# Performance work log

Hardware: AMD Instinct MI355X
Metric: run time of the kernel (lower is better)

The kernel has to match this reference:

```python
import jax, jax.numpy as jnp
import numpy as np

def setup_inputs() -> dict:
    key = jax.random.key(0)
    x = jax.random.normal(key, (4096, 3, 64, 64), dtype=jnp.float32)
    return {"x": x}

def reference(x):
    # x: [N, C=3, H, W]; attention runs over the N dim with feature dim H*W
    N, C, H, W = x.shape
    out = x.reshape(N, C, H * W)          # [N, 3, HW]
    q, k, v = out[:, 0], out[:, 1], out[:, 2]  # each [N, HW]
    dp = (q @ k.T) * 0.5                  # [N, N]
    attn = jax.nn.softmax(dp, axis=-1)
    # dropout omitted (eval-mode / deterministic reference)
    return attn @ v                       # [N, HW]
```

## Files before the change

kernel.cpp:

```cpp
#include <hip/hip_runtime.h>
#include <hip/hip_bf16.h>
#include <cstdint>

#define N 4096
#define ROWSTRIDE 12288

typedef __attribute__((ext_vector_type(8))) _Float16 half8;
typedef __attribute__((ext_vector_type(4))) _Float16 half4v;
typedef __attribute__((ext_vector_type(4))) float floatx4;

__global__ __launch_bounds__(256) void pack_qk(const float* __restrict__ x,
                                               _Float16* __restrict__ qh,
                                               _Float16* __restrict__ kh) {
    const size_t tid = (size_t)blockIdx.x * 256 + threadIdx.x;
    const int i  = (int)(tid >> 10);
    const int c4 = (int)(tid & 1023);
    const float4* xr = (const float4*)(x + (size_t)i * ROWSTRIDE);
    float4 q = xr[c4];
    float4 k = xr[1024 + c4];
    half4v qo = {(_Float16)(q.x * 0.5f), (_Float16)(q.y * 0.5f),
                 (_Float16)(q.z * 0.5f), (_Float16)(q.w * 0.5f)};
    half4v ko = {(_Float16)k.x, (_Float16)k.y, (_Float16)k.z, (_Float16)k.w};
    *(half4v*)(qh + tid * 4) = qo;
    *(half4v*)(kh + tid * 4) = ko;
}

__global__ __launch_bounds__(256) void transpose_v(const float* __restrict__ x,
                                                   _Float16* __restrict__ vt) {
    __shared__ float tile[32][33];
    const int j0 = blockIdx.x * 32;
    const int d0 = blockIdx.y * 32;
    const int t  = threadIdx.x;
    const int r  = t >> 3;
    const int c4 = t & 7;
    const float4 val = *(const float4*)(x + (size_t)(j0 + r) * ROWSTRIDE + 8192 + d0 + c4 * 4);
    tile[r][c4 * 4 + 0] = val.x;
    tile[r][c4 * 4 + 1] = val.y;
    tile[r][c4 * 4 + 2] = val.z;
    tile[r][c4 * 4 + 3] = val.w;
    __syncthreads();
    half4v o = {(_Float16)tile[c4 * 4 + 0][r], (_Float16)tile[c4 * 4 + 1][r],
                (_Float16)tile[c4 * 4 + 2][r], (_Float16)tile[c4 * 4 + 3][r]};
    *(half4v*)(vt + (size_t)(d0 + r) * N + j0 + c4 * 4) = o;
}

#define GL2LDS(g, l)                                                                     \
    __builtin_amdgcn_global_load_lds((const __attribute__((address_space(1))) void*)(g), \
                                     (__attribute__((address_space(3))) void*)(l), 16, 0, 0)

__global__ __launch_bounds__(512, 2) void gemm_nt256(const _Float16* __restrict__ A,
                                                     const _Float16* __restrict__ Bt,
                                                     float* __restrict__ C) {
    __shared__ _Float16 lds[65536];
    const int t    = threadIdx.x;
    const int wave = t >> 6;
    const int lane = t & 63;
    const int wr   = wave >> 2;
    const int wc   = wave & 3;

    const int orig = blockIdx.y * 16 + blockIdx.x;
    const int wg   = (orig & 7) * 32 + (orig >> 3);
    const int rowBase = (wg >> 4) * 256;
    const int colBase = (wg & 15) * 256;

    floatx4 acc[8][4] = {};

    const int sRow = t >> 2;
    const int sCg  = (t & 3) ^ ((t >> 3) & 3);
    const _Float16* gA = A  + (size_t)(rowBase + sRow) * N + sCg * 8;
    const _Float16* gB = Bt + (size_t)(colBase + sRow) * N + sCg * 8;
    const int ldsW = wave * 512;

    const int fr   = lane & 15;
    const int quad = lane >> 4;
    const int swc  = quad ^ ((fr >> 1) & 3);
    const int rdA  = (wr * 128 + fr) * 32 + swc * 8;
    const int rdB  = (wc * 64 + fr) * 32 + swc * 8;

#define STAGE(regOff, g, kOff)                                                  \
    do {                                                                        \
        GL2LDS((g) + (kOff), &lds[(regOff) + ldsW]);                            \
        GL2LDS((g) + (kOff) + (size_t)128 * N, &lds[(regOff) + 4096 + ldsW]);   \
    } while (0)

    STAGE(0, gA, 0);
    STAGE(8192, gB, 0);
    STAGE(16384, gA, 32);
    STAGE(24576, gB, 32);
    asm volatile("s_waitcnt vmcnt(4)" ::: "memory");
    __builtin_amdgcn_s_barrier();

    for (int kt = 0; kt < 63; ++kt) {
        const int rb = (kt & 1) * 32768;
        const int sb = rb ^ 32768;
        const int kNext = (kt + 1) * 64;
#pragma unroll
        for (int kh = 0; kh < 2; ++kh) {
            const int rA = rb + kh * 16384;
            const int rB = rA + 8192;
            half8 af[4], bf[4];
#pragma unroll
            for (int nt = 0; nt < 4; ++nt) bf[nt] = *(const half8*)&lds[rB + nt * 512 + rdB];
#pragma unroll
            for (int mt = 0; mt < 4; ++mt) af[mt] = *(const half8*)&lds[rA + mt * 512 + rdA];
            STAGE(sb + kh * 16384, gA, kNext + kh * 32);
            __builtin_amdgcn_s_barrier();
            asm volatile("s_waitcnt lgkmcnt(0)" ::: "memory");
            __builtin_amdgcn_s_setprio(1);
#pragma unroll
            for (int mt = 0; mt < 4; ++mt)
#pragma unroll
                for (int nt = 0; nt < 4; ++nt)
                    acc[mt][nt] = __builtin_amdgcn_mfma_f32_16x16x32_f16(af[mt], bf[nt],
                                                                         acc[mt][nt], 0, 0, 0);
            __builtin_amdgcn_s_setprio(0);
            __builtin_amdgcn_s_barrier();
#pragma unroll
            for (int mt = 0; mt < 4; ++mt) af[mt] = *(const half8*)&lds[rA + (mt + 4) * 512 + rdA];
            STAGE(sb + kh * 16384 + 8192, gB, kNext + kh * 32);
            asm volatile("s_waitcnt vmcnt(4)" ::: "memory");
            __builtin_amdgcn_s_barrier();
            asm volatile("s_waitcnt lgkmcnt(0)" ::: "memory");
            __builtin_amdgcn_s_setprio(1);
#pragma unroll
            for (int mt = 0; mt < 4; ++mt)
#pragma unroll
                for (int nt = 0; nt < 4; ++nt)
                    acc[mt + 4][nt] = __builtin_amdgcn_mfma_f32_16x16x32_f16(af[mt], bf[nt],
                                                                             acc[mt + 4][nt], 0, 0, 0);
            __builtin_amdgcn_s_setprio(0);
            __builtin_amdgcn_s_barrier();
        }
    }

    {
        const int rb = 32768;
#pragma unroll
        for (int kh = 0; kh < 2; ++kh) {
            const int rA = rb + kh * 16384;
            const int rB = rA + 8192;
            half8 af[4], bf[4];
#pragma unroll
            for (int nt = 0; nt < 4; ++nt) bf[nt] = *(const half8*)&lds[rB + nt * 512 + rdB];
#pragma unroll
            for (int mt = 0; mt < 4; ++mt) af[mt] = *(const half8*)&lds[rA + mt * 512 + rdA];
            __builtin_amdgcn_s_barrier();
            asm volatile("s_waitcnt lgkmcnt(0)" ::: "memory");
            __builtin_amdgcn_s_setprio(1);
#pragma unroll
            for (int mt = 0; mt < 4; ++mt)
#pragma unroll
                for (int nt = 0; nt < 4; ++nt)
                    acc[mt][nt] = __builtin_amdgcn_mfma_f32_16x16x32_f16(af[mt], bf[nt],
                                                                         acc[mt][nt], 0, 0, 0);
            __builtin_amdgcn_s_setprio(0);
            __builtin_amdgcn_s_barrier();
#pragma unroll
            for (int mt = 0; mt < 4; ++mt) af[mt] = *(const half8*)&lds[rA + (mt + 4) * 512 + rdA];
            if (kh == 0) asm volatile("s_waitcnt vmcnt(0)" ::: "memory");
            __builtin_amdgcn_s_barrier();
            asm volatile("s_waitcnt lgkmcnt(0)" ::: "memory");
            __builtin_amdgcn_s_setprio(1);
#pragma unroll
            for (int mt = 0; mt < 4; ++mt)
#pragma unroll
                for (int nt = 0; nt < 4; ++nt)
                    acc[mt + 4][nt] = __builtin_amdgcn_mfma_f32_16x16x32_f16(af[mt], bf[nt],
                                                                             acc[mt + 4][nt], 0, 0, 0);
            __builtin_amdgcn_s_setprio(0);
            __builtin_amdgcn_s_barrier();
        }
    }

#pragma unroll
    for (int mt = 0; mt < 8; ++mt) {
#pragma unroll
        for (int nt = 0; nt < 4; ++nt) {
#pragma unroll
            for (int r = 0; r < 4; ++r) {
                const int row = rowBase + wr * 128 + mt * 16 + quad * 4 + r;
                const int col = colBase + wc * 64 + nt * 16 + fr;
                C[(size_t)row * N + col] = acc[mt][nt][r];
            }
        }
    }
#undef STAGE
}

__global__ __launch_bounds__(256) void softmax_rows(const float* __restrict__ S,
                                                    _Float16* __restrict__ P) {
    const int row = blockIdx.x;
    const int t   = threadIdx.x;
    const float4* Sr = (const float4*)(S + (size_t)row * N);

    float4 v[4];
    float lmax = -3.0e38f;
#pragma unroll
    for (int r = 0; r < 4; ++r) {
        v[r] = Sr[t + 256 * r];
        lmax = fmaxf(lmax, fmaxf(fmaxf(v[r].x, v[r].y), fmaxf(v[r].z, v[r].w)));
    }
#pragma unroll
    for (int off = 32; off; off >>= 1) lmax = fmaxf(lmax, __shfl_xor(lmax, off, 64));
    __shared__ float redm[4], reds[4];
    const int wave = t >> 6, lane = t & 63;
    if (lane == 0) redm[wave] = lmax;
    __syncthreads();
    const float m = fmaxf(fmaxf(redm[0], redm[1]), fmaxf(redm[2], redm[3]));

    float lsum = 0.f;
#pragma unroll
    for (int r = 0; r < 4; ++r) {
        v[r].x = __expf(v[r].x - m);
        v[r].y = __expf(v[r].y - m);
        v[r].z = __expf(v[r].z - m);
        v[r].w = __expf(v[r].w - m);
        lsum += (v[r].x + v[r].y) + (v[r].z + v[r].w);
    }
#pragma unroll
    for (int off = 32; off; off >>= 1) lsum += __shfl_xor(lsum, off, 64);
    if (lane == 0) reds[wave] = lsum;
    __syncthreads();
    const float inv = 1.0f / (((reds[0] + reds[1]) + (reds[2] + reds[3])));

#pragma unroll
    for (int r = 0; r < 4; ++r) {
        half4v o = {(_Float16)(v[r].x * inv), (_Float16)(v[r].y * inv),
                    (_Float16)(v[r].z * inv), (_Float16)(v[r].w * inv)};
        *(half4v*)(P + (size_t)row * N + (t + 256 * r) * 4) = o;
    }
}

extern "C" void kernel_launch(void* const* d_in, const int* in_sizes, int n_in,
                              void* d_out, int out_size, void* d_ws, size_t ws_size,
                              hipStream_t stream) {
    const float* x = (const float*)d_in[0];
    float* out     = (float*)d_out;
    char* ws       = (char*)d_ws;

    _Float16* qh = (_Float16*)(ws);
    _Float16* kh = (_Float16*)(ws + (32ull << 20));
    _Float16* vt = (_Float16*)(ws + (64ull << 20));
    float*    S  = (float*)   (ws + (96ull << 20));
    _Float16* P  = qh;

    pack_qk     <<<16384, 256, 0, stream>>>(x, qh, kh);
    transpose_v <<<dim3(128, 128), 256, 0, stream>>>(x, vt);
    gemm_nt256  <<<dim3(16, 16), 512, 0, stream>>>(qh, kh, S);
    softmax_rows<<<4096, 256, 0, stream>>>(S, P);
    gemm_nt256  <<<dim3(16, 16), 512, 0, stream>>>(P, vt, out);
}
```

Baseline: 546.7 us.

## Drop post-MFMA barriers in GEMM and widen pack/transpose stores to half8

Removes the workgroup barrier after each MFMA block in both the main and tail loops of the GEMM. The aim is to cut synchronisation stalls so waves can begin the next fragment loads and staging sooner. The pack_qk and transpose_v kernels are also changed to handle twice the data per thread and write 16-byte half8 stores, which halves their grid sizes. The risk is an LDS race: the pipeline's buffer reuse may have depended on the removed barriers.

Measured after the change: 529.5 us. 1.03x faster.

```diff
diff --git a/kernel.cpp b/kernel.cpp
--- a/kernel.cpp
+++ b/kernel.cpp
@@ -13,35 +13,45 @@
                                                _Float16* __restrict__ qh,
                                                _Float16* __restrict__ kh) {
     const size_t tid = (size_t)blockIdx.x * 256 + threadIdx.x;
-    const int i  = (int)(tid >> 10);
-    const int c4 = (int)(tid & 1023);
+    const int i  = (int)(tid >> 9);
+    const int c8 = (int)(tid & 511);
     const float4* xr = (const float4*)(x + (size_t)i * ROWSTRIDE);
-    float4 q = xr[c4];
-    float4 k = xr[1024 + c4];
-    half4v qo = {(_Float16)(q.x * 0.5f), (_Float16)(q.y * 0.5f),
-                 (_Float16)(q.z * 0.5f), (_Float16)(q.w * 0.5f)};
-    half4v ko = {(_Float16)k.x, (_Float16)k.y, (_Float16)k.z, (_Float16)k.w};
-    *(half4v*)(qh + tid * 4) = qo;
-    *(half4v*)(kh + tid * 4) = ko;
+    float4 qa = xr[c8 * 2], qb = xr[c8 * 2 + 1];
+    float4 ka = xr[1024 + c8 * 2], kb = xr[1024 + c8 * 2 + 1];
+    half8 qo = {(_Float16)(qa.x * 0.5f), (_Float16)(qa.y * 0.5f),
+                (_Float16)(qa.z * 0.5f), (_Float16)(qa.w * 0.5f),
+                (_Float16)(qb.x * 0.5f), (_Float16)(qb.y * 0.5f),
+                (_Float16)(qb.z * 0.5f), (_Float16)(qb.w * 0.5f)};
+    half8 ko = {(_Float16)ka.x, (_Float16)ka.y, (_Float16)ka.z, (_Float16)ka.w,
+                (_Float16)kb.x, (_Float16)kb.y, (_Float16)kb.z, (_Float16)kb.w};
+    *(half8*)(qh + (size_t)i * N + c8 * 8) = qo;
+    *(half8*)(kh + (size_t)i * N + c8 * 8) = ko;
 }
 
 __global__ __launch_bounds__(256) void transpose_v(const float* __restrict__ x,
                                                    _Float16* __restrict__ vt) {
-    __shared__ float tile[32][33];
+    __shared__ float tile[32][65];
     const int j0 = blockIdx.x * 32;
-    const int d0 = blockIdx.y * 32;
+    const int d0 = blockIdx.y * 64;
     const int t  = threadIdx.x;
-    const int r  = t >> 3;
-    const int c4 = t & 7;
-    const float4 val = *(const float4*)(x + (size_t)(j0 + r) * ROWSTRIDE + 8192 + d0 + c4 * 4);
-    tile[r][c4 * 4 + 0] = val.x;
-    tile[r][c4 * 4 + 1] = val.y;
-    tile[r][c4 * 4 + 2] = val.z;
-    tile[r][c4 * 4 + 3] = val.w;
+#pragma unroll
+    for (int it = 0; it < 2; ++it) {
+        const int r  = it * 16 + (t >> 4);
+        const int c4 = t & 15;
+        const float4 val =
+            *(const float4*)(x + (size_t)(j0 + r) * ROWSTRIDE + 8192 + d0 + c4 * 4);
+        tile[r][c4 * 4 + 0] = val.x;
+        tile[r][c4 * 4 + 1] = val.y;
+        tile[r][c4 * 4 + 2] = val.z;
+        tile[r][c4 * 4 + 3] = val.w;
+    }
     __syncthreads();
-    half4v o = {(_Float16)tile[c4 * 4 + 0][r], (_Float16)tile[c4 * 4 + 1][r],
-                (_Float16)tile[c4 * 4 + 2][r], (_Float16)tile[c4 * 4 + 3][r]};
-    *(half4v*)(vt + (size_t)(d0 + r) * N + j0 + c4 * 4) = o;
+    const int dr = t >> 2;
+    const int jc = t & 3;
+    half8 o;
+#pragma unroll
+    for (int jj = 0; jj < 8; ++jj) o[jj] = (_Float16)tile[jc * 8 + jj][dr];
+    *(half8*)(vt + (size_t)(d0 + dr) * N + j0 + jc * 8) = o;
 }
 
 #define GL2LDS(g, l)                                                                     \
@@ -114,7 +124,6 @@
                     acc[mt][nt] = __builtin_amdgcn_mfma_f32_16x16x32_f16(af[mt], bf[nt],
                                                                          acc[mt][nt], 0, 0, 0);
             __builtin_amdgcn_s_setprio(0);
-            __builtin_amdgcn_s_barrier();
 #pragma unroll
             for (int mt = 0; mt < 4; ++mt) af[mt] = *(const half8*)&lds[rA + (mt + 4) * 512 + rdA];
             STAGE(sb + kh * 16384 + 8192, gB, kNext + kh * 32);
@@ -129,7 +138,6 @@
                     acc[mt + 4][nt] = __builtin_amdgcn_mfma_f32_16x16x32_f16(af[mt], bf[nt],
                                                                              acc[mt + 4][nt], 0, 0, 0);
             __builtin_amdgcn_s_setprio(0);
-            __builtin_amdgcn_s_barrier();
         }
     }
 
@@ -154,7 +162,6 @@
                     acc[mt][nt] = __builtin_amdgcn_mfma_f32_16x16x32_f16(af[mt], bf[nt],
                                                                          acc[mt][nt], 0, 0, 0);
             __builtin_amdgcn_s_setprio(0);
-            __builtin_amdgcn_s_barrier();
 #pragma unroll
             for (int mt = 0; mt < 4; ++mt) af[mt] = *(const half8*)&lds[rA + (mt + 4) * 512 + rdA];
             if (kh == 0) asm volatile("s_waitcnt vmcnt(0)" ::: "memory");
@@ -168,7 +175,6 @@
                     acc[mt + 4][nt] = __builtin_amdgcn_mfma_f32_16x16x32_f16(af[mt], bf[nt],
                                                                              acc[mt + 4][nt], 0, 0, 0);
             __builtin_amdgcn_s_setprio(0);
-            __builtin_amdgcn_s_barrier();
         }
     }
 
@@ -244,8 +250,8 @@
     float*    S  = (float*)   (ws + (96ull << 20));
     _Float16* P  = qh;
 
-    pack_qk     <<<16384, 256, 0, stream>>>(x, qh, kh);
-    transpose_v <<<dim3(128, 128), 256, 0, stream>>>(x, vt);
+    pack_qk     <<<8192, 256, 0, stream>>>(x, qh, kh);
+    transpose_v <<<dim3(128, 64), 256, 0, stream>>>(x, vt);
     gemm_nt256  <<<dim3(16, 16), 512, 0, stream>>>(qh, kh, S);
     softmax_rows<<<4096, 256, 0, stream>>>(S, P);
     gemm_nt256  <<<dim3(16, 16), 512, 0, stream>>>(P, vt, out);
```
